# Optimization experiments

Measured on AMD Instinct MI355X. Metric: run time of the kernel, lower is better.

## Reference

```python
import jax, jax.numpy as jnp
import numpy as np

N_NODES = 100000
D_IN = 256
D_HID = 64
D_EMB = 32
ADJ_NNZ = 3200000
N_EDGES = 2000000


def setup_inputs() -> dict:
    key = jax.random.key(0)
    ks = jax.random.split(key, 8)
    x = jax.random.normal(ks[0], (N_NODES, D_IN), dtype=jnp.float32)
    adj_src = jax.random.randint(ks[1], (ADJ_NNZ,), 0, N_NODES, dtype=jnp.int32)
    adj_dst = jax.random.randint(ks[2], (ADJ_NNZ,), 0, N_NODES, dtype=jnp.int32)
    adj_val = jax.random.uniform(ks[3], (ADJ_NNZ,), dtype=jnp.float32)
    edge_index = jax.random.randint(ks[4], (2, N_EDGES), 0, N_NODES, dtype=jnp.int32)
    # Xavier-uniform weights, zero biases (matches reset_parameters)
    lim1 = float(np.sqrt(6.0 / (D_IN + D_HID)))
    lim2 = float(np.sqrt(6.0 / (D_HID + D_EMB)))
    W1 = jax.random.uniform(ks[5], (D_IN, D_HID), minval=-lim1, maxval=lim1, dtype=jnp.float32)
    b1 = jnp.zeros((D_HID,), dtype=jnp.float32)
    W2 = jax.random.uniform(ks[6], (D_HID, D_EMB), minval=-lim2, maxval=lim2, dtype=jnp.float32)
    b2 = jnp.zeros((D_EMB,), dtype=jnp.float32)
    return {"x": x, "adj_src": adj_src, "adj_dst": adj_dst, "adj_val": adj_val,
            "edge_index": edge_index, "W1": W1, "b1": b1, "W2": W2, "b2": b2}


def _spmm(adj_src, adj_dst, adj_val, dense):
    # (sparse A) @ dense : out[i] = sum_{e: dst[e]==i} val[e] * dense[src[e]]
    n = dense.shape[0]
    msgs = adj_val[:, None] * dense[adj_src]            # [nnz, d]
    return jax.ops.segment_sum(msgs, adj_dst, num_segments=n)


def reference(x, adj_src, adj_dst, adj_val, edge_index, W1, b1, W2, b2):
    # Layer 1: ReLU(A_norm @ (x W1) + b1)
    z1 = jax.nn.relu(_spmm(adj_src, adj_dst, adj_val, x @ W1) + b1)
    # Layer 2: A_norm @ (z1 W2) + b2 (no activation)
    z2 = _spmm(adj_src, adj_dst, adj_val, z1 @ W2) + b2   # [n, d_emb]
    # Inner-product decoder over edges
    src, dst = edge_index[0], edge_index[1]
    scores = jnp.sum(z2[src] * z2[dst], axis=1)          # [num_edges]
    return scores
```

## Files before the change

### kernel.cpp

```cpp
#include <hip/hip_runtime.h>
#include <hip/hip_bf16.h>


#define D_IN  256
#define D_HID 64
#define D_EMB 32
#define BROWS 256
#define NBUK_MAX 512
#define TILE  4096
#define PBS   512
#define SBS   1024

typedef unsigned short u16;
typedef unsigned int u32;
typedef __attribute__((ext_vector_type(8))) short short8;
typedef __attribute__((ext_vector_type(4))) float f32x4;

__device__ __forceinline__ float bf2f(u32 u) {
  return __uint_as_float((u & 0xFFFFu) << 16);
}
__device__ __forceinline__ float bf2f_hi(u32 u) {
  return __uint_as_float(u & 0xFFFF0000u);
}
__device__ __forceinline__ u16 f2bf(float f) {
  u32 x = __float_as_uint(f);
  x += 0x7FFFu + ((x >> 16) & 1u);
  return (u16)(x >> 16);
}
__device__ __forceinline__ void unpack8(uint4 u, float* f) {
  f[0] = bf2f(u.x); f[1] = bf2f(u.x >> 16);
  f[2] = bf2f(u.y); f[3] = bf2f(u.y >> 16);
  f[4] = bf2f(u.z); f[5] = bf2f(u.z >> 16);
  f[6] = bf2f(u.w); f[7] = bf2f(u.w >> 16);
}

__global__ __launch_bounds__(256) void w1_swizzle_kernel(
    const float* __restrict__ W1, uint4* __restrict__ gswz) {
  const int s = blockIdx.x * 256 + threadIdx.x;
  const int lane = s & 63;
  const int kstep = (s >> 6) & 7;
  const int nt = s >> 9;
  const int col = nt * 16 + (lane & 15);
  const int kbase = kstep * 32 + (lane >> 4) * 8;
  u32 p[4];
  for (int jp = 0; jp < 4; ++jp) {
    u32 lo = f2bf(W1[(kbase + 2 * jp) * D_HID + col]);
    u32 hi = f2bf(W1[(kbase + 2 * jp + 1) * D_HID + col]);
    p[jp] = lo | (hi << 16);
  }
  gswz[s] = make_uint4(p[0], p[1], p[2], p[3]);
}

__global__ __launch_bounds__(256) void bin_count(
    const int* __restrict__ dst, int* __restrict__ hist, int nnz, int nbuk) {
  __shared__ int h[NBUK_MAX];
  for (int i = threadIdx.x; i < nbuk; i += 256) h[i] = 0;
  __syncthreads();
  const int stride = gridDim.x * 256;
  for (int e = blockIdx.x * 256 + threadIdx.x; e < nnz; e += stride)
    atomicAdd(&h[dst[e] >> 8], 1);
  __syncthreads();
  for (int i = threadIdx.x; i < nbuk; i += 256) {
    int v = h[i];
    if (v) atomicAdd(&hist[i], v);
  }
}

__global__ __launch_bounds__(256) void bin_scan(
    int* __restrict__ hist, int* __restrict__ cur, int n) {
  __shared__ int sm[256];
  const int t = threadIdx.x;
  const int per = (n + 255) / 256;
  const int base = t * per;
  int loc[4];
  int s = 0;
  for (int i = 0; i < per; ++i) {
    int idx = base + i;
    int v = (idx < n) ? hist[idx] : 0;
    loc[i] = s;
    s += v;
  }
  sm[t] = s;
  __syncthreads();
  for (int off = 1; off < 256; off <<= 1) {
    int tmp = (t >= off) ? sm[t - off] : 0;
    __syncthreads();
    sm[t] += tmp;
    __syncthreads();
  }
  const int b0 = sm[t] - s;
  for (int i = 0; i < per; ++i) {
    int idx = base + i;
    if (idx < n) {
      int p = b0 + loc[i];
      hist[idx] = p;
      cur[idx] = p;
    }
  }
  if (t == 255) hist[n] = sm[255];
}

__global__ __launch_bounds__(PBS) void partition_kernel(
    const int* __restrict__ src, const int* __restrict__ dst,
    const float* __restrict__ val, int* __restrict__ cur,
    int2* __restrict__ payload, int nnz, int nbuk) {
  __shared__ int2 stage[TILE];
  __shared__ int hist[NBUK_MAX];
  __shared__ int lcur[NBUK_MAX];
  __shared__ int gbase[NBUK_MAX];
  __shared__ int sm[PBS];

  const int t = threadIdx.x;
  const long long base = (long long)blockIdx.x * TILE;
  const int cnt = min(TILE, (int)(nnz - base));

  for (int i = t; i < nbuk; i += PBS) hist[i] = 0;
  __syncthreads();

  constexpr int PER = TILE / PBS;
  int key[PER], vq[PER];
  short bk[PER];
  for (int i = 0; i < PER; ++i) {
    int idx = t + i * PBS;
    if (idx < cnt) {
      int d = dst[base + idx];
      int b = d >> 8;
      bk[i] = (short)b;
      key[i] = (src[base + idx] << 8) | (d & (BROWS - 1));
      int q = (int)(val[base + idx] * 32768.f + 0.5f);
      q = min(q, 32767);
      vq[i] = (b << 15) | q;
      atomicAdd(&hist[b], 1);
    } else {
      bk[i] = -1;
    }
  }
  __syncthreads();

  {
    int c = (t < nbuk) ? hist[t] : 0;
    sm[t] = c;
    __syncthreads();
    for (int off = 1; off < PBS; off <<= 1) {
      int tmp = (t >= off) ? sm[t - off] : 0;
      __syncthreads();
      sm[t] += tmp;
      __syncthreads();
    }
    int excl = sm[t] - c;
    if (t < nbuk) {
      hist[t] = excl;
      lcur[t] = excl;
      if (c > 0) gbase[t] = atomicAdd(&cur[t], c);
    }
  }
  __syncthreads();

  for (int i = 0; i < PER; ++i) {
    if (bk[i] >= 0) {
      int p = atomicAdd(&lcur[bk[i]], 1);
      stage[p] = make_int2(key[i], vq[i]);
    }
  }
  __syncthreads();

  for (int i = t; i < cnt; i += PBS) {
    int2 pk = stage[i];
    int b = pk.y >> 15;
    payload[gbase[b] + (i - hist[b])] = pk;
  }
}

__global__ __launch_bounds__(SBS) void bucket_sort_kernel(
    const int* __restrict__ bscan, const int2* __restrict__ payload,
    u32* __restrict__ csr, int* __restrict__ rs, int M) {
  __shared__ int cnt_s[BROWS];
  __shared__ int sm[BROWS];
  const int b = blockIdx.x;
  const int t = threadIdx.x;
  const int start = bscan[b];
  const int end = bscan[b + 1];

  if (t < BROWS) cnt_s[t] = 0;
  __syncthreads();
  for (int j = start + t; j < end; j += SBS)
    atomicAdd(&cnt_s[payload[j].x & (BROWS - 1)], 1);
  __syncthreads();

  int v = 0;
  if (t < BROWS) { v = cnt_s[t]; sm[t] = v; }
  __syncthreads();
  for (int off = 1; off < BROWS; off <<= 1) {
    int tmp = 0;
    if (t < BROWS && t >= off) tmp = sm[t - off];
    __syncthreads();
    if (t < BROWS) sm[t] += tmp;
    __syncthreads();
  }
  if (t < BROWS) {
    int row = b * BROWS + t;
    if (row < M) rs[row] = start + sm[t];
    cnt_s[t] = start + sm[t] - v;
  }
  __syncthreads();

  for (int j = start + t; j < end; j += SBS) {
    int2 pk = payload[j];
    int r = pk.x & (BROWS - 1);
    int p = atomicAdd(&cnt_s[r], 1);
    csr[p] = ((u32)(pk.x >> 8) << 15) | (u32)(pk.y & 32767);
  }
}

__global__ __launch_bounds__(256) void gemm1_mfma_kernel(
    const float* __restrict__ x, const uint4* __restrict__ gswz,
    u16* __restrict__ h1, int M) {
  const int tid = threadIdx.x;
  const int wv = tid >> 6;
  const int lane = tid & 63;
  const int quad = lane >> 4;
  const int m = lane & 15;

  const int rowbase = blockIdx.x * 64 + wv * 16;
  int arow = rowbase + m;
  if (arow >= M) arow = M - 1;

  f32x4 acc[4];
  for (int nt = 0; nt < 4; ++nt) acc[nt] = (f32x4){0.f, 0.f, 0.f, 0.f};

  const float* xrow = &x[(long long)arow * D_IN];

#pragma unroll
  for (int kstep = 0; kstep < 8; ++kstep) {
    const int kbase = kstep * 32 + quad * 8;
    float4 a0 = *(const float4*)&xrow[kbase];
    float4 a1 = *(const float4*)&xrow[kbase + 4];
    short8 af;
    af[0] = (short)f2bf(a0.x); af[1] = (short)f2bf(a0.y);
    af[2] = (short)f2bf(a0.z); af[3] = (short)f2bf(a0.w);
    af[4] = (short)f2bf(a1.x); af[5] = (short)f2bf(a1.y);
    af[6] = (short)f2bf(a1.z); af[7] = (short)f2bf(a1.w);
#pragma unroll
    for (int nt = 0; nt < 4; ++nt) {
      uint4 bu = gswz[(nt * 8 + kstep) * 64 + lane];
      short8 bf = *(short8*)&bu;
      acc[nt] = __builtin_amdgcn_mfma_f32_16x16x32_bf16(af, bf, acc[nt], 0, 0, 0);
    }
  }

#pragma unroll
  for (int nt = 0; nt < 4; ++nt) {
#pragma unroll
    for (int r = 0; r < 4; ++r) {
      int orow = rowbase + quad * 4 + r;
      if (orow < M)
        h1[(long long)orow * D_HID + nt * 16 + m] = f2bf(acc[nt][r]);
    }
  }
}

template <int D, bool RELU>
__global__ __launch_bounds__(256) void spmm_csr_kernel(
    const int* __restrict__ rs, const u32* __restrict__ csr,
    const u16* __restrict__ in, const float* __restrict__ bias,
    u16* __restrict__ out, int M) {
  constexpr int TEAM = D / 4;
  constexpr int SH = (D == 64) ? 6 : 5;
  const int lt = threadIdx.x % TEAM;
  const int row = blockIdx.x * (256 / TEAM) + threadIdx.x / TEAM;
  if (row >= M) return;
  const int start = (row == 0) ? 0 : rs[row - 1];
  const int end = rs[row];
  const float qs = 1.f / 32768.f;
  const u16* inp = in + lt * 4;

  float a0 = 0.f, a1 = 0.f, a2 = 0.f, a3 = 0.f;
  int j = start;

  int head = (4 - (start & 3)) & 3;
  if (head > end - start) head = end - start;
  for (int h = 0; h < head; ++h, ++j) {
    u32 pk = csr[j];
    uint2 w = *(const uint2*)(inp + ((pk >> 15) << SH));
    float v = (float)(pk & 32767u) * qs;
    a0 = fmaf(v, bf2f(w.x), a0); a1 = fmaf(v, bf2f_hi(w.x), a1);
    a2 = fmaf(v, bf2f(w.y), a2); a3 = fmaf(v, bf2f_hi(w.y), a3);
  }

  for (; j + 8 <= end; j += 8) {
    uint4 pa = *(const uint4*)&csr[j];
    uint4 pb = *(const uint4*)&csr[j + 4];
    uint2 w0 = *(const uint2*)(inp + ((pa.x >> 15) << SH));
    uint2 w1 = *(const uint2*)(inp + ((pa.y >> 15) << SH));
    uint2 w2 = *(const uint2*)(inp + ((pa.z >> 15) << SH));
    uint2 w3 = *(const uint2*)(inp + ((pa.w >> 15) << SH));
    uint2 w4 = *(const uint2*)(inp + ((pb.x >> 15) << SH));
    uint2 w5 = *(const uint2*)(inp + ((pb.y >> 15) << SH));
    uint2 w6 = *(const uint2*)(inp + ((pb.z >> 15) << SH));
    uint2 w7 = *(const uint2*)(inp + ((pb.w >> 15) << SH));
    float v0 = (float)(pa.x & 32767u) * qs;
    float v1 = (float)(pa.y & 32767u) * qs;
    float v2 = (float)(pa.z & 32767u) * qs;
    float v3 = (float)(pa.w & 32767u) * qs;
    float v4 = (float)(pb.x & 32767u) * qs;
    float v5 = (float)(pb.y & 32767u) * qs;
    float v6 = (float)(pb.z & 32767u) * qs;
    float v7 = (float)(pb.w & 32767u) * qs;
    a0 = fmaf(v0, bf2f(w0.x), a0); a1 = fmaf(v0, bf2f_hi(w0.x), a1);
    a2 = fmaf(v0, bf2f(w0.y), a2); a3 = fmaf(v0, bf2f_hi(w0.y), a3);
    a0 = fmaf(v1, bf2f(w1.x), a0); a1 = fmaf(v1, bf2f_hi(w1.x), a1);
    a2 = fmaf(v1, bf2f(w1.y), a2); a3 = fmaf(v1, bf2f_hi(w1.y), a3);
    a0 = fmaf(v2, bf2f(w2.x), a0); a1 = fmaf(v2, bf2f_hi(w2.x), a1);
    a2 = fmaf(v2, bf2f(w2.y), a2); a3 = fmaf(v2, bf2f_hi(w2.y), a3);
    a0 = fmaf(v3, bf2f(w3.x), a0); a1 = fmaf(v3, bf2f_hi(w3.x), a1);
    a2 = fmaf(v3, bf2f(w3.y), a2); a3 = fmaf(v3, bf2f_hi(w3.y), a3);
    a0 = fmaf(v4, bf2f(w4.x), a0); a1 = fmaf(v4, bf2f_hi(w4.x), a1);
    a2 = fmaf(v4, bf2f(w4.y), a2); a3 = fmaf(v4, bf2f_hi(w4.y), a3);
    a0 = fmaf(v5, bf2f(w5.x), a0); a1 = fmaf(v5, bf2f_hi(w5.x), a1);
    a2 = fmaf(v5, bf2f(w5.y), a2); a3 = fmaf(v5, bf2f_hi(w5.y), a3);
    a0 = fmaf(v6, bf2f(w6.x), a0); a1 = fmaf(v6, bf2f_hi(w6.x), a1);
    a2 = fmaf(v6, bf2f(w6.y), a2); a3 = fmaf(v6, bf2f_hi(w6.y), a3);
    a0 = fmaf(v7, bf2f(w7.x), a0); a1 = fmaf(v7, bf2f_hi(w7.x), a1);
    a2 = fmaf(v7, bf2f(w7.y), a2); a3 = fmaf(v7, bf2f_hi(w7.y), a3);
  }

  for (; j + 4 <= end; j += 4) {
    uint4 p = *(const uint4*)&csr[j];
    uint2 w0 = *(const uint2*)(inp + ((p.x >> 15) << SH));
    uint2 w1 = *(const uint2*)(inp + ((p.y >> 15) << SH));
    uint2 w2 = *(const uint2*)(inp + ((p.z >> 15) << SH));
    uint2 w3 = *(const uint2*)(inp + ((p.w >> 15) << SH));
    float v0 = (float)(p.x & 32767u) * qs;
    float v1 = (float)(p.y & 32767u) * qs;
    float v2 = (float)(p.z & 32767u) * qs;
    float v3 = (float)(p.w & 32767u) * qs;
    a0 = fmaf(v0, bf2f(w0.x), a0); a1 = fmaf(v0, bf2f_hi(w0.x), a1);
    a2 = fmaf(v0, bf2f(w0.y), a2); a3 = fmaf(v0, bf2f_hi(w0.y), a3);
    a0 = fmaf(v1, bf2f(w1.x), a0); a1 = fmaf(v1, bf2f_hi(w1.x), a1);
    a2 = fmaf(v1, bf2f(w1.y), a2); a3 = fmaf(v1, bf2f_hi(w1.y), a3);
    a0 = fmaf(v2, bf2f(w2.x), a0); a1 = fmaf(v2, bf2f_hi(w2.x), a1);
    a2 = fmaf(v2, bf2f(w2.y), a2); a3 = fmaf(v2, bf2f_hi(w2.y), a3);
    a0 = fmaf(v3, bf2f(w3.x), a0); a1 = fmaf(v3, bf2f_hi(w3.x), a1);
    a2 = fmaf(v3, bf2f(w3.y), a2); a3 = fmaf(v3, bf2f_hi(w3.y), a3);
  }
  for (; j < end; ++j) {
    u32 pk = csr[j];
    uint2 w = *(const uint2*)(inp + ((pk >> 15) << SH));
    float v = (float)(pk & 32767u) * qs;
    a0 = fmaf(v, bf2f(w.x), a0); a1 = fmaf(v, bf2f_hi(w.x), a1);
    a2 = fmaf(v, bf2f(w.y), a2); a3 = fmaf(v, bf2f_hi(w.y), a3);
  }
  const float4 bv = *(const float4*)&bias[lt * 4];
  a0 += bv.x; a1 += bv.y; a2 += bv.z; a3 += bv.w;
  if (RELU) {
    a0 = fmaxf(a0, 0.f); a1 = fmaxf(a1, 0.f);
    a2 = fmaxf(a2, 0.f); a3 = fmaxf(a3, 0.f);
  }
  uint2 o;
  o.x = (u32)f2bf(a0) | ((u32)f2bf(a1) << 16);
  o.y = (u32)f2bf(a2) | ((u32)f2bf(a3) << 16);
  *(uint2*)&out[((u32)row << SH) + lt * 4] = o;
}

__global__ __launch_bounds__(256) void gemm2_kernel(
    const u16* __restrict__ z1, const float* __restrict__ W2,
    u16* __restrict__ h2, int M) {
  __shared__ float wsm[D_HID * D_EMB];
  const int tid = threadIdx.x;
  for (int i = tid; i < D_HID * D_EMB / 4; i += 256)
    ((float4*)wsm)[i] = ((const float4*)W2)[i];
  __syncthreads();

  const int row = blockIdx.x * 256 + tid;
  if (row >= M) return;

  float4 acc4[8];
  for (int c = 0; c < 8; ++c) acc4[c] = make_float4(0.f, 0.f, 0.f, 0.f);

  const uint4* zr = (const uint4*)&z1[(long long)row * D_HID];
  for (int blk = 0; blk < 8; ++blk) {
    float a8[8];
    unpack8(zr[blk], a8);
    for (int kk = 0; kk < 8; ++kk) {
      const float a = a8[kk];
      const float4* wr = (const float4*)&wsm[(blk * 8 + kk) * D_EMB];
      for (int c = 0; c < 8; ++c) {
        float4 wv = wr[c];
        acc4[c].x += a * wv.x;
        acc4[c].y += a * wv.y;
        acc4[c].z += a * wv.z;
        acc4[c].w += a * wv.w;
      }
    }
  }
  u32 pk[16];
  for (int c = 0; c < 8; ++c) {
    pk[c * 2 + 0] = (u32)f2bf(acc4[c].x) | ((u32)f2bf(acc4[c].y) << 16);
    pk[c * 2 + 1] = (u32)f2bf(acc4[c].z) | ((u32)f2bf(acc4[c].w) << 16);
  }
  uint4* op = (uint4*)&h2[(long long)row * D_EMB];
  op[0] = make_uint4(pk[0], pk[1], pk[2], pk[3]);
  op[1] = make_uint4(pk[4], pk[5], pk[6], pk[7]);
  op[2] = make_uint4(pk[8], pk[9], pk[10], pk[11]);
  op[3] = make_uint4(pk[12], pk[13], pk[14], pk[15]);
}

__global__ __launch_bounds__(256) void decode_kernel(
    const int* __restrict__ ei, const u16* __restrict__ z2,
    float* __restrict__ out, int nE) {
  const int t = blockIdx.x * 256 + threadIdx.x;
  const int e0 = t * 2;
  if (e0 >= nE) return;
  const bool two = (e0 + 1 < nE);

  const int2 ss = *(const int2*)&ei[e0];
  const int2 dd = *(const int2*)&ei[nE + e0];

  const uint4* za = (const uint4*)(z2 + ((u32)ss.x << 5));
  const uint4* zb = (const uint4*)(z2 + ((u32)dd.x << 5));
  const uint4* zc = (const uint4*)(z2 + ((u32)(two ? ss.y : ss.x) << 5));
  const uint4* zd = (const uint4*)(z2 + ((u32)(two ? dd.y : dd.x) << 5));

  uint4 A[2], B[2], C[2], Dv[2];
  A[0] = za[0]; A[1] = za[1];
  B[0] = zb[0]; B[1] = zb[1];
  C[0] = zc[0]; C[1] = zc[1];
  Dv[0] = zd[0]; Dv[1] = zd[1];
  uint4 A2[2], B2[2], C2[2], D2[2];
  A2[0] = za[2]; A2[1] = za[3];
  B2[0] = zb[2]; B2[1] = zb[3];
  C2[0] = zc[2]; C2[1] = zc[3];
  D2[0] = zd[2]; D2[1] = zd[3];

  float acc0 = 0.f, acc1 = 0.f;
  float a8[8], b8[8];
#pragma unroll
  for (int c = 0; c < 2; ++c) {
    unpack8(A[c], a8); unpack8(B[c], b8);
#pragma unroll
    for (int k = 0; k < 8; ++k) acc0 = fmaf(a8[k], b8[k], acc0);
    unpack8(A2[c], a8); unpack8(B2[c], b8);
#pragma unroll
    for (int k = 0; k < 8; ++k) acc0 = fmaf(a8[k], b8[k], acc0);
    unpack8(C[c], a8); unpack8(Dv[c], b8);
#pragma unroll
    for (int k = 0; k < 8; ++k) acc1 = fmaf(a8[k], b8[k], acc1);
    unpack8(C2[c], a8); unpack8(D2[c], b8);
#pragma unroll
    for (int k = 0; k < 8; ++k) acc1 = fmaf(a8[k], b8[k], acc1);
  }
  out[e0] = acc0;
  if (two) out[e0 + 1] = acc1;
}

extern "C" void kernel_launch(void* const* d_in, const int* in_sizes, int n_in,
                              void* d_out, int out_size, void* d_ws, size_t ws_size,
                              hipStream_t stream) {
  const float* x       = (const float*)d_in[0];
  const int*   adj_src = (const int*)d_in[1];
  const int*   adj_dst = (const int*)d_in[2];
  const float* adj_val = (const float*)d_in[3];
  const int*   ei      = (const int*)d_in[4];
  const float* W1      = (const float*)d_in[5];
  const float* b1      = (const float*)d_in[6];
  const float* W2      = (const float*)d_in[7];
  const float* b2      = (const float*)d_in[8];

  const int M   = in_sizes[0] / D_IN;
  const int nnz = in_sizes[1];
  const int nE  = in_sizes[4] / 2;

  const int NBUK = (M + BROWS - 1) / BROWS;

  char* ws = (char*)d_ws;
  u32*   csr     = (u32*)(ws);
  int2*  payload = (int2*)(ws + (size_t)nnz * 4);
  u16*   h1      = (u16*)(ws + (size_t)nnz * 4);
  u16*   z1      = (u16*)(ws + (size_t)nnz * 4 + (size_t)nnz * 8);
  u16*   h2      = h1;
  u16*   z2      = z1;
  uint4* gswz    = (uint4*)(ws + 60ull * 1024 * 1024);

  int* rs    = (int*)d_out;
  int* bscan = (int*)d_out + 112 * 1024;
  int* cur   = (int*)d_out + 120 * 1024;

  w1_swizzle_kernel<<<8, 256, 0, stream>>>(W1, gswz);

  hipMemsetAsync(bscan, 0, (size_t)(NBUK + 1) * 4, stream);
  bin_count<<<256, 256, 0, stream>>>(adj_dst, bscan, nnz, NBUK);
  bin_scan<<<1, 256, 0, stream>>>(bscan, cur, NBUK);
  partition_kernel<<<(nnz + TILE - 1) / TILE, PBS, 0, stream>>>(
      adj_src, adj_dst, adj_val, cur, payload, nnz, NBUK);

  bucket_sort_kernel<<<NBUK, SBS, 0, stream>>>(bscan, payload, csr, rs, M);

  gemm1_mfma_kernel<<<(M + 63) / 64, 256, 0, stream>>>(x, gswz, h1, M);

  spmm_csr_kernel<D_HID, true><<<(M + 15) / 16, 256, 0, stream>>>(
      rs, csr, h1, b1, z1, M);

  gemm2_kernel<<<(M + 255) / 256, 256, 0, stream>>>(z1, W2, h2, M);

  spmm_csr_kernel<D_EMB, false><<<(M + 31) / 32, 256, 0, stream>>>(
      rs, csr, h2, b2, z2, M);

  decode_kernel<<<(nE / 2 + 255) / 256, 256, 0, stream>>>(ei, z2, (float*)d_out, nE);
}
```

Measured before the change: 433.6 us.

## Fuse layer-1 SpMM with the W2 GEMM into one kernel

```diff
diff --git a/kernel.cpp b/kernel.cpp
--- a/kernel.cpp
+++ b/kernel.cpp
@@ -257,6 +257,133 @@
         h1[(long long)orow * D_HID + nt * 16 + m] = f2bf(acc[nt][r]);
     }
   }
+}
+
+__global__ __launch_bounds__(256) void spmm1_gemm2_fused(
+    const int* __restrict__ rs, const u32* __restrict__ csr,
+    const u16* __restrict__ in, const float* __restrict__ b1,
+    const float* __restrict__ W2, u16* __restrict__ h2, int M) {
+  __shared__ float w2s[D_HID * D_EMB];
+  __shared__ float z1s[16][68];
+
+  const int tid = threadIdx.x;
+  for (int i = tid; i < D_HID * D_EMB / 4; i += 256)
+    ((float4*)w2s)[i] = ((const float4*)W2)[i];
+  __syncthreads();
+
+  const int lt = tid & 15;
+  const int tb = tid >> 4;
+  const int row = blockIdx.x * 16 + tb;
+  if (row >= M) return;
+
+  const int start = (row == 0) ? 0 : rs[row - 1];
+  const int end = rs[row];
+  const float qs = 1.f / 32768.f;
+  const u16* inp = in + lt * 4;
+
+  float a0 = 0.f, a1 = 0.f, a2 = 0.f, a3 = 0.f;
+  int j = start;
+
+  int head = (4 - (start & 3)) & 3;
+  if (head > end - start) head = end - start;
+  for (int h = 0; h < head; ++h, ++j) {
+    u32 pk = csr[j];
+    uint2 w = *(const uint2*)(inp + ((pk >> 15) << 6));
+    float v = (float)(pk & 32767u) * qs;
+    a0 = fmaf(v, bf2f(w.x), a0); a1 = fmaf(v, bf2f_hi(w.x), a1);
+    a2 = fmaf(v, bf2f(w.y), a2); a3 = fmaf(v, bf2f_hi(w.y), a3);
+  }
+
+  for (; j + 8 <= end; j += 8) {
+    uint4 pa = *(const uint4*)&csr[j];
+    uint4 pb = *(const uint4*)&csr[j + 4];
+    uint2 w0 = *(const uint2*)(inp + ((pa.x >> 15) << 6));
+    uint2 w1 = *(const uint2*)(inp + ((pa.y >> 15) << 6));
+    uint2 w2 = *(const uint2*)(inp + ((pa.z >> 15) << 6));
+    uint2 w3 = *(const uint2*)(inp + ((pa.w >> 15) << 6));
+    uint2 w4 = *(const uint2*)(inp + ((pb.x >> 15) << 6));
+    uint2 w5 = *(const uint2*)(inp + ((pb.y >> 15) << 6));
+    uint2 w6 = *(const uint2*)(inp + ((pb.z >> 15) << 6));
+    uint2 w7 = *(const uint2*)(inp + ((pb.w >> 15) << 6));
+    float v0 = (float)(pa.x & 32767u) * qs;
+    float v1 = (float)(pa.y & 32767u) * qs;
+    float v2 = (float)(pa.z & 32767u) * qs;
+    float v3 = (float)(pa.w & 32767u) * qs;
+    float v4 = (float)(pb.x & 32767u) * qs;
+    float v5 = (float)(pb.y & 32767u) * qs;
+    float v6 = (float)(pb.z & 32767u) * qs;
+    float v7 = (float)(pb.w & 32767u) * qs;
+    a0 = fmaf(v0, bf2f(w0.x), a0); a1 = fmaf(v0, bf2f_hi(w0.x), a1);
+    a2 = fmaf(v0, bf2f(w0.y), a2); a3 = fmaf(v0, bf2f_hi(w0.y), a3);
+    a0 = fmaf(v1, bf2f(w1.x), a0); a1 = fmaf(v1, bf2f_hi(w1.x), a1);
+    a2 = fmaf(v1, bf2f(w1.y), a2); a3 = fmaf(v1, bf2f_hi(w1.y), a3);
+    a0 = fmaf(v2, bf2f(w2.x), a0); a1 = fmaf(v2, bf2f_hi(w2.x), a1);
+    a2 = fmaf(v2, bf2f(w2.y), a2); a3 = fmaf(v2, bf2f_hi(w2.y), a3);
+    a0 = fmaf(v3, bf2f(w3.x), a0); a1 = fmaf(v3, bf2f_hi(w3.x), a1);
+    a2 = fmaf(v3, bf2f(w3.y), a2); a3 = fmaf(v3, bf2f_hi(w3.y), a3);
+    a0 = fmaf(v4, bf2f(w4.x), a0); a1 = fmaf(v4, bf2f_hi(w4.x), a1);
+    a2 = fmaf(v4, bf2f(w4.y), a2); a3 = fmaf(v4, bf2f_hi(w4.y), a3);
+    a0 = fmaf(v5, bf2f(w5.x), a0); a1 = fmaf(v5, bf2f_hi(w5.x), a1);
+    a2 = fmaf(v5, bf2f(w5.y), a2); a3 = fmaf(v5, bf2f_hi(w5.y), a3);
+    a0 = fmaf(v6, bf2f(w6.x), a0); a1 = fmaf(v6, bf2f_hi(w6.x), a1);
+    a2 = fmaf(v6, bf2f(w6.y), a2); a3 = fmaf(v6, bf2f_hi(w6.y), a3);
+    a0 = fmaf(v7, bf2f(w7.x), a0); a1 = fmaf(v7, bf2f_hi(w7.x), a1);
+    a2 = fmaf(v7, bf2f(w7.y), a2); a3 = fmaf(v7, bf2f_hi(w7.y), a3);
+  }
+
+  for (; j + 4 <= end; j += 4) {
+    uint4 p = *(const uint4*)&csr[j];
+    uint2 w0 = *(const uint2*)(inp + ((p.x >> 15) << 6));
+    uint2 w1 = *(const uint2*)(inp + ((p.y >> 15) << 6));
+    uint2 w2 = *(const uint2*)(inp + ((p.z >> 15) << 6));
+    uint2 w3 = *(const uint2*)(inp + ((p.w >> 15) << 6));
+    float v0 = (float)(p.x & 32767u) * qs;
+    float v1 = (float)(p.y & 32767u) * qs;
+    float v2 = (float)(p.z & 32767u) * qs;
+    float v3 = (float)(p.w & 32767u) * qs;
+    a0 = fmaf(v0, bf2f(w0.x), a0); a1 = fmaf(v0, bf2f_hi(w0.x), a1);
+    a2 = fmaf(v0, bf2f(w0.y), a2); a3 = fmaf(v0, bf2f_hi(w0.y), a3);
+    a0 = fmaf(v1, bf2f(w1.x), a0); a1 = fmaf(v1, bf2f_hi(w1.x), a1);
+    a2 = fmaf(v1, bf2f(w1.y), a2); a3 = fmaf(v1, bf2f_hi(w1.y), a3);
+    a0 = fmaf(v2, bf2f(w2.x), a0); a1 = fmaf(v2, bf2f_hi(w2.x), a1);
+    a2 = fmaf(v2, bf2f(w2.y), a2); a3 = fmaf(v2, bf2f_hi(w2.y), a3);
+    a0 = fmaf(v3, bf2f(w3.x), a0); a1 = fmaf(v3, bf2f_hi(w3.x), a1);
+    a2 = fmaf(v3, bf2f(w3.y), a2); a3 = fmaf(v3, bf2f_hi(w3.y), a3);
+  }
+  for (; j < end; ++j) {
+    u32 pk = csr[j];
+    uint2 w = *(const uint2*)(inp + ((pk >> 15) << 6));
+    float v = (float)(pk & 32767u) * qs;
+    a0 = fmaf(v, bf2f(w.x), a0); a1 = fmaf(v, bf2f_hi(w.x), a1);
+    a2 = fmaf(v, bf2f(w.y), a2); a3 = fmaf(v, bf2f_hi(w.y), a3);
+  }
+
+  const float4 bv = *(const float4*)&b1[lt * 4];
+  a0 = fmaxf(a0 + bv.x, 0.f);
+  a1 = fmaxf(a1 + bv.y, 0.f);
+  a2 = fmaxf(a2 + bv.z, 0.f);
+  a3 = fmaxf(a3 + bv.w, 0.f);
+
+  float* zrow = z1s[tb];
+  zrow[lt * 4 + 0] = a0;
+  zrow[lt * 4 + 1] = a1;
+  zrow[lt * 4 + 2] = a2;
+  zrow[lt * 4 + 3] = a3;
+  float h0 = 0.f, h1v = 0.f;
+#pragma unroll
+  for (int k = 0; k < D_HID; k += 4) {
+    float4 z4 = *(const float4*)&zrow[k];
+    h0  = fmaf(z4.x, w2s[(k + 0) * D_EMB + 2 * lt], h0);
+    h1v = fmaf(z4.x, w2s[(k + 0) * D_EMB + 2 * lt + 1], h1v);
+    h0  = fmaf(z4.y, w2s[(k + 1) * D_EMB + 2 * lt], h0);
+    h1v = fmaf(z4.y, w2s[(k + 1) * D_EMB + 2 * lt + 1], h1v);
+    h0  = fmaf(z4.z, w2s[(k + 2) * D_EMB + 2 * lt], h0);
+    h1v = fmaf(z4.z, w2s[(k + 2) * D_EMB + 2 * lt + 1], h1v);
+    h0  = fmaf(z4.w, w2s[(k + 3) * D_EMB + 2 * lt], h0);
+    h1v = fmaf(z4.w, w2s[(k + 3) * D_EMB + 2 * lt + 1], h1v);
+  }
+  u32 o = (u32)f2bf(h0) | ((u32)f2bf(h1v) << 16);
+  ((u32*)h2)[((u32)row << 4) + lt] = o;
 }
 
 template <int D, bool RELU>
@@ -362,49 +489,6 @@
   *(uint2*)&out[((u32)row << SH) + lt * 4] = o;
 }
 
-__global__ __launch_bounds__(256) void gemm2_kernel(
-    const u16* __restrict__ z1, const float* __restrict__ W2,
-    u16* __restrict__ h2, int M) {
-  __shared__ float wsm[D_HID * D_EMB];
-  const int tid = threadIdx.x;
-  for (int i = tid; i < D_HID * D_EMB / 4; i += 256)
-    ((float4*)wsm)[i] = ((const float4*)W2)[i];
-  __syncthreads();
-
-  const int row = blockIdx.x * 256 + tid;
-  if (row >= M) return;
-
-  float4 acc4[8];
-  for (int c = 0; c < 8; ++c) acc4[c] = make_float4(0.f, 0.f, 0.f, 0.f);
-
-  const uint4* zr = (const uint4*)&z1[(long long)row * D_HID];
-  for (int blk = 0; blk < 8; ++blk) {
-    float a8[8];
-    unpack8(zr[blk], a8);
-    for (int kk = 0; kk < 8; ++kk) {
-      const float a = a8[kk];
-      const float4* wr = (const float4*)&wsm[(blk * 8 + kk) * D_EMB];
-      for (int c = 0; c < 8; ++c) {
-        float4 wv = wr[c];
-        acc4[c].x += a * wv.x;
-        acc4[c].y += a * wv.y;
-        acc4[c].z += a * wv.z;
-        acc4[c].w += a * wv.w;
-      }
-    }
-  }
-  u32 pk[16];
-  for (int c = 0; c < 8; ++c) {
-    pk[c * 2 + 0] = (u32)f2bf(acc4[c].x) | ((u32)f2bf(acc4[c].y) << 16);
-    pk[c * 2 + 1] = (u32)f2bf(acc4[c].z) | ((u32)f2bf(acc4[c].w) << 16);
-  }
-  uint4* op = (uint4*)&h2[(long long)row * D_EMB];
-  op[0] = make_uint4(pk[0], pk[1], pk[2], pk[3]);
-  op[1] = make_uint4(pk[4], pk[5], pk[6], pk[7]);
-  op[2] = make_uint4(pk[8], pk[9], pk[10], pk[11]);
-  op[3] = make_uint4(pk[12], pk[13], pk[14], pk[15]);
-}
-
 __global__ __launch_bounds__(256) void decode_kernel(
     const int* __restrict__ ei, const u16* __restrict__ z2,
     float* __restrict__ out, int nE) {
@@ -476,9 +560,8 @@
   u32*   csr     = (u32*)(ws);
   int2*  payload = (int2*)(ws + (size_t)nnz * 4);
   u16*   h1      = (u16*)(ws + (size_t)nnz * 4);
-  u16*   z1      = (u16*)(ws + (size_t)nnz * 4 + (size_t)nnz * 8);
-  u16*   h2      = h1;
-  u16*   z2      = z1;
+  u16*   h2      = (u16*)(ws + (size_t)nnz * 4 + (size_t)M * D_HID * 2);
+  u16*   z2      = (u16*)(ws + (size_t)nnz * 12);
   uint4* gswz    = (uint4*)(ws + 60ull * 1024 * 1024);
 
   int* rs    = (int*)d_out;
@@ -497,10 +580,8 @@
 
   gemm1_mfma_kernel<<<(M + 63) / 64, 256, 0, stream>>>(x, gswz, h1, M);
 
-  spmm_csr_kernel<D_HID, true><<<(M + 15) / 16, 256, 0, stream>>>(
-      rs, csr, h1, b1, z1, M);
-
-  gemm2_kernel<<<(M + 255) / 256, 256, 0, stream>>>(z1, W2, h2, M);
+  spmm1_gemm2_fused<<<(M + 15) / 16, 256, 0, stream>>>(
+      rs, csr, h1, b1, W2, h2, M);
 
   spmm_csr_kernel<D_EMB, false><<<(M + 31) / 32, 256, 0, stream>>>(
       rs, csr, h2, b2, z2, M);
```

New measurement: 417.5 us. -3.7%, faster.
